# Kernel optimization log

Hardware: AMD Instinct MI355X
Metric: run time of the kernel (lower is better)

Reference implementation:

```python
import jax, jax.numpy as jnp
import numpy as np

N = 100000   # nodes
E = 800000   # edges (avg degree 8)
C = 64       # channels
IN_A = 512
IN_V = 512
EPS = 1e-5
BN_SCALE = float(1.0 / np.sqrt(1.0 + EPS))  # eval-mode BN with rm=0, rv=1


def setup_inputs() -> dict:
    key = jax.random.key(0)
    ks = jax.random.split(key, 24)
    s = 0.05
    rnd = lambda k, shp: jax.random.normal(k, shp, jnp.float32)
    inp = {}
    inp["x"] = rnd(ks[0], (N, 2, IN_A))
    inp["edge_index"] = jax.random.randint(ks[1], (2, E), 0, N, dtype=jnp.int32)
    inp["edge_delta"] = jax.random.randint(ks[2], (E,), 0, 30, dtype=jnp.int32)
    inp["edge_self"] = jax.random.randint(ks[3], (E,), 0, 2, dtype=jnp.int32)
    inp["audio_node_mask"] = (jnp.arange(N) % 2) == 0
    # layer_0 linear projections
    inp["W0a"] = rnd(ks[4], (IN_A, C)) * s
    inp["b0a"] = rnd(ks[5], (C,)) * s
    inp["W0v"] = rnd(ks[6], (IN_V, C)) * s
    inp["b0v"] = rnd(ks[7], (C,)) * s
    # batch_0 affine
    inp["bn0_g"] = 1.0 + rnd(ks[8], (C,)) * s
    inp["bn0_b"] = rnd(ks[9], (C,)) * s
    # 4 EdgeConv LinearPathPreact blocks (stacked along leading axis)
    inp["ec_bn1_g"] = 1.0 + rnd(ks[10], (4, 2 * C)) * s
    inp["ec_bn1_b"] = rnd(ks[11], (4, 2 * C)) * s
    inp["ec_fc1_W"] = rnd(ks[12], (4, 2 * C, C)) * s
    inp["ec_bn2_g"] = 1.0 + rnd(ks[13], (4, C)) * s
    inp["ec_bn2_b"] = rnd(ks[14], (4, C)) * s
    inp["ec_fc2_W"] = rnd(ks[15], (4, C, C)) * s
    # batch_1..batch_3 affines
    inp["bn_g"] = 1.0 + rnd(ks[16], (3, C)) * s
    inp["bn_b"] = rnd(ks[17], (3, C)) * s
    # heads
    inp["fca_W"] = rnd(ks[18], (C, 2)) * s
    inp["fca_b"] = rnd(ks[19], (2,)) * s
    inp["fcv_W"] = rnd(ks[20], (C, 2)) * s
    inp["fcv_b"] = rnd(ks[21], (2,)) * s
    inp["fc_W"] = rnd(ks[22], (C, 2)) * s
    inp["fc_b"] = rnd(ks[23], (2,)) * s
    return inp


def _bn(x, g, b):
    # eval-mode BatchNorm1d with running_mean=0, running_var=1
    return x * (BN_SCALE * g) + b


def _lpp(m, g1, b1, W1, g2, b2, W2):
    # LinearPathPreact: BN -> ReLU -> Linear -> BN -> ReLU -> Linear (no biases)
    h = jnp.maximum(_bn(m, g1, b1), 0.0) @ W1
    return jnp.maximum(_bn(h, g2, b2), 0.0) @ W2


def _edgeconv(xf, src, dst, maskf, g1, b1, W1, g2, b2, W2):
    # PyG EdgeConv: message = nn(cat([x_i, x_j - x_i])), mean-aggregated at dst i.
    # Distance-mask is applied as a 0/1 edge weight with masked mean (no dynamic shapes).
    xi = xf[dst]              # [E, C]
    xj = xf[src]              # [E, C]
    msg = _lpp(jnp.concatenate([xi, xj - xi], axis=-1), g1, b1, W1, g2, b2, W2)
    msg = msg * maskf[:, None]
    cnt = jax.ops.segment_sum(maskf, dst, num_segments=N)
    acc = jax.ops.segment_sum(msg, dst, num_segments=N)
    return acc / jnp.maximum(cnt, 1.0)[:, None]


def reference(x, edge_index, edge_delta, edge_self, audio_node_mask,
              W0a, b0a, W0v, b0v, bn0_g, bn0_b,
              ec_bn1_g, ec_bn1_b, ec_fc1_W, ec_bn2_g, ec_bn2_b, ec_fc2_W,
              bn_g, bn_b, fca_W, fca_b, fcv_W, fcv_b, fc_W, fc_b):
    src, dst = edge_index[0], edge_index[1]
    # only the first two distance masks are used in the original forward
    m1 = (edge_delta < 1).astype(x.dtype)
    m2 = (((edge_delta >= 1) & (edge_delta < 4)) | (edge_self == 1)).astype(x.dtype)

    a_out = x[:, 0, :IN_A] @ W0a + b0a
    v_out = x[:, 1, :IN_V] @ W0v + b0v
    gf = jnp.where(audio_node_mask[:, None], a_out, v_out)
    gf = jnp.maximum(_bn(gf, bn0_g, bn0_b), 0.0)

    def block(xin, k):
        p = (ec_bn1_g[k], ec_bn1_b[k], ec_fc1_W[k], ec_bn2_g[k], ec_bn2_b[k], ec_fc2_W[k])
        h = _edgeconv(xin, src, dst, m1, *p)
        return _edgeconv(h, src, dst, m2, *p)

    g1 = jnp.maximum(_bn(block(gf, 0), bn_g[0], bn_b[0]), 0.0)   # dropout is eval-mode identity
    g2 = jnp.maximum(_bn(block(g1, 1) + g1, bn_g[1], bn_b[1]), 0.0)
    g3 = jnp.maximum(_bn(block(g2, 2) + g2, bn_g[2], bn_b[2]), 0.0)
    g4 = block(g3, 3) + g3

    out = g4 @ fc_W + fc_b
    audio_out = gf[audio_node_mask] @ fca_W + fca_b
    video_out = gf[~audio_node_mask] @ fcv_W + fcv_b
    return (out, audio_out, video_out)
```

## Files before the change

### kernel.cpp

```cpp
#include <hip/hip_runtime.h>


#define NN 100000
#define NE 800000
#define NB 391
#define BNS 0.9999950000374998f

typedef __attribute__((ext_vector_type(8))) short short8;
typedef __attribute__((ext_vector_type(4))) float f32x4;

__device__ __forceinline__ float bf_lo(unsigned u){ union{unsigned i; float f;} v; v.i = u << 16; return v.f; }
__device__ __forceinline__ float bf_hi(unsigned u){ union{unsigned i; float f;} v; v.i = u & 0xffff0000u; return v.f; }
__device__ __forceinline__ float bf2f(unsigned short u){ union{unsigned i; float f;} v; v.i = ((unsigned)u) << 16; return v.f; }
__device__ __forceinline__ unsigned short f2bf(float f){
  union{float f; unsigned i;} v; v.f = f;
  unsigned r = v.i + 0x7fffu + ((v.i >> 16) & 1u);
  return (unsigned short)(r >> 16);
}
__device__ __forceinline__ unsigned packbf(float a, float b){
  return (unsigned)f2bf(a) | ((unsigned)f2bf(b) << 16);
}


__global__ __launch_bounds__(256) void hist_kernel(
    const int* __restrict__ ei, const int* __restrict__ edel,
    const int* __restrict__ esel, int* cnt1, int* cnt2)
{
  int e = blockIdx.x * 256 + threadIdx.x;
  if (e >= NE) return;
  int d = edel[e], s = esel[e], dst = ei[NE + e];
  if (d < 1) atomicAdd(cnt1 + dst, 1);
  if ((d >= 1 && d < 4) || s == 1) atomicAdd(cnt2 + dst, 1);
}

__global__ __launch_bounds__(256) void scan1_kernel(
    const int* __restrict__ cnt1, const int* __restrict__ cnt2,
    int* row1, int* row2, int* bsum)
{
  const int a = blockIdx.y;
  const int* cnt = a ? cnt2 : cnt1;
  int* row = a ? row2 : row1;
  int t = threadIdx.x, b = blockIdx.x, i = b * 256 + t;
  int v = (i < NN) ? cnt[i] : 0;
  __shared__ int sc[256];
  sc[t] = v; __syncthreads();
#pragma unroll
  for (int off = 1; off < 256; off <<= 1){
    int x = (t >= off) ? sc[t - off] : 0;
    __syncthreads();
    sc[t] += x;
    __syncthreads();
  }
  if (i < NN) row[i] = sc[t] - v;
  if (t == 255) bsum[a * 400 + b] = sc[t];
}

__global__ __launch_bounds__(512) void scan2_kernel(int* bsum, int* boff, int* ctr)
{
  int t = threadIdx.x;
  __shared__ int sc[512];
  for (int a = 0; a < 2; a++){
    int v = (t < NB) ? bsum[a * 400 + t] : 0;
    __syncthreads();
    sc[t] = v; __syncthreads();
#pragma unroll
    for (int off = 1; off < 512; off <<= 1){
      int x = (t >= off) ? sc[t - off] : 0;
      __syncthreads();
      sc[t] += x;
      __syncthreads();
    }
    if (t < NB) boff[a * 400 + t] = sc[t] - v;
    if (t == NB - 1) ctr[a] = sc[t];
  }
}

__global__ __launch_bounds__(256) void scan3_kernel(
    int* row1, int* row2, int* cur1, int* cur2, const int* __restrict__ boff)
{
  const int a = blockIdx.y;
  int* row = a ? row2 : row1;
  int* cur = a ? cur2 : cur1;
  int i = blockIdx.x * 256 + threadIdx.x;
  if (i >= NN) return;
  int r = row[i] + boff[a * 400 + blockIdx.x];
  row[i] = r;
  cur[i] = r;
}

__global__ __launch_bounds__(256) void inv_kernel(
    const int* __restrict__ cnt1, const int* __restrict__ cnt2,
    float* inv1, float* inv2)
{
  int i = blockIdx.x * 256 + threadIdx.x;
  if (i >= NN) return;
  inv1[i] = 1.f / fmaxf((float)cnt1[i], 1.f);
  inv2[i] = 1.f / fmaxf((float)cnt2[i], 1.f);
}

__global__ __launch_bounds__(256) void compact_kernel(
    const int* __restrict__ ei, const int* __restrict__ edel,
    const int* __restrict__ esel, int* cur1, int* cur2,
    int* s1s, int* s2s)
{
  int e = blockIdx.x * 256 + threadIdx.x;
  if (e >= NE) return;
  int d = edel[e], s = esel[e], src = ei[e], dst = ei[NE + e];
  int rec = src | ((dst & 15) << 20);
  if (d < 1){ int p = atomicAdd(cur1 + dst, 1); s1s[p] = rec; }
  if ((d >= 1 && d < 4) || s == 1){ int p = atomicAdd(cur2 + dst, 1); s2s[p] = rec; }
}

__global__ __launch_bounds__(256) void prep_w(
    const float* __restrict__ W1, const float* __restrict__ W2,
    const float* __restrict__ g1, const float* __restrict__ g2,
    const float* __restrict__ b1,
    unsigned short* __restrict__ wf1, unsigned short* __restrict__ wf2,
    float* __restrict__ t1p)
{
  int g = blockIdx.x * 256 + threadIdx.x;
  if (g >= 6656) return;
  if (g >= 6144){
    int i = g - 6144;
    int k = i >> 7, c = i & 127;
    t1p[i] = b1[k * 128 + c] / (BNS * g1[k * 128 + c]);
    return;
  }
  int k = g / 1536, r = g % 1536, f = r >> 6, l = r & 63;
  int q = l >> 4, m = l & 15;
  if (f < 16){
    int t = f >> 2, h = f & 3;
    unsigned short* o = wf1 + (((size_t)k * 16 + f) * 64 + l) * 8;
    const float* Wk = W1 + k * 8192;
    int cp = t * 16 + m;
    float cs = BNS * g2[k * 64 + cp];
#pragma unroll
    for (int j = 0; j < 8; j++){
      int kg = h * 32 + q * 8 + j;
      float w, rs;
      if (kg < 64){
        w  = Wk[(64 + kg) * 64 + cp];
        rs = BNS * g1[k * 128 + 64 + kg];
      } else {
        w  = Wk[(kg - 64) * 64 + cp];
        rs = BNS * g1[k * 128 + kg - 64];
      }
      o[j] = f2bf(w * rs * cs);
    }
  } else {
    int f2 = f - 16, t = f2 >> 1, h = f2 & 1;
    unsigned short* o = wf2 + (((size_t)k * 8 + f2) * 64 + l) * 8;
    const float* Wk = W2 + k * 4096;
#pragma unroll
    for (int j = 0; j < 8; j++){
      int kg = h * 32 + q * 8 + j;
      o[j] = f2bf(Wk[kg * 64 + t * 16 + m]);
    }
  }
}

__global__ __launch_bounds__(256) void prep_w0(
    const float* __restrict__ W0a, const float* __restrict__ W0v,
    unsigned short* __restrict__ wf0)
{
  int g = blockIdx.x * 256 + threadIdx.x;
  if (g >= 8192) return;
  int l = g & 63, t = (g >> 6) & 3, ks = (g >> 8) & 15, tt = (g >> 12) & 1;
  const float* W = tt ? W0v : W0a;
  int c = t * 16 + (l & 15);
  int kb = ks * 32 + (l >> 4) * 8;
  unsigned short* o = wf0 + (size_t)g * 8;
#pragma unroll
  for (int j = 0; j < 8; j++) o[j] = f2bf(W[(kb + j) * 64 + c]);
}


__global__ __launch_bounds__(256) void s0_kernel(
    const float* __restrict__ x,
    const float* __restrict__ b0a, const float* __restrict__ b0v,
    const float* __restrict__ bn0g, const float* __restrict__ bn0b,
    const unsigned short* __restrict__ wf0,
    unsigned short* __restrict__ Xb)
{
  const int tt = blockIdx.y;
  const int wv = threadIdx.x >> 6;
  const int l  = threadIdx.x & 63;
  const int q = l >> 4, m16 = l & 15;
  const int wid = blockIdx.x * 4 + wv;
  if (wid >= 3125) return;
  const int node = wid * 16 + m16;
  const float* bias = tt ? b0v : b0a;

  float fs[4][4], ft[4][4];
#pragma unroll
  for (int t = 0; t < 4; t++)
#pragma unroll
    for (int r = 0; r < 4; r++){
      int c = t * 16 + q * 4 + r;
      float s = BNS * bn0g[c];
      fs[t][r] = s;
      ft[t][r] = bias[c] * s + bn0b[c];
    }

  const unsigned short* wbase = wf0 + (size_t)tt * 16 * 4 * 64 * 8;
  const float* xp = x + (size_t)(2 * node + tt) * 1024 + tt * 512 + q * 8;

  f32x4 acc[4];
#pragma unroll
  for (int t = 0; t < 4; t++) acc[t] = (f32x4){0.f, 0.f, 0.f, 0.f};

  for (int ks = 0; ks < 16; ks++){
    float4 xa = *(const float4*)(xp + ks * 32);
    float4 xb = *(const float4*)(xp + ks * 32 + 4);
    union { unsigned u[4]; short8 s; } bb;
    bb.u[0] = packbf(xa.x, xa.y);
    bb.u[1] = packbf(xa.z, xa.w);
    bb.u[2] = packbf(xb.x, xb.y);
    bb.u[3] = packbf(xb.z, xb.w);
    const unsigned short* wk = wbase + (size_t)ks * 4 * 64 * 8 + l * 8;
#pragma unroll
    for (int t = 0; t < 4; t++){
      short8 a = *(const short8*)(wk + t * 64 * 8);
      acc[t] = __builtin_amdgcn_mfma_f32_16x16x32_bf16(a, bb.s, acc[t], 0, 0, 0);
    }
  }

  const int i = 2 * node + tt;
  unsigned short* op = Xb + (size_t)i * 64 + (q << 2);
#pragma unroll
  for (int t = 0; t < 4; t++){
    float v0 = fmaxf(fmaf(acc[t][0], fs[t][0], ft[t][0]), 0.f);
    float v1 = fmaxf(fmaf(acc[t][1], fs[t][1], ft[t][1]), 0.f);
    float v2 = fmaxf(fmaf(acc[t][2], fs[t][2], ft[t][2]), 0.f);
    float v3 = fmaxf(fmaf(acc[t][3], fs[t][3], ft[t][3]), 0.f);
    uint2 w; w.x = packbf(v0, v1); w.y = packbf(v2, v3);
    *(uint2*)(op + t * 16) = w;
  }
}


__global__ __launch_bounds__(256, 3) void edge_pass(
    const unsigned short* __restrict__ fin,
    const int* __restrict__ spk,
    const int* __restrict__ row, const int* __restrict__ cnt,
    const float* __restrict__ inv,
    const unsigned short* __restrict__ wf1,
    const unsigned short* __restrict__ wf2,
    const float* __restrict__ t1p,
    const float* __restrict__ bn2b,
    const unsigned short* resid,
    const float* __restrict__ bng, const float* __restrict__ bnb,
    unsigned short* __restrict__ outb, int hasres, int hasbn)
{
  const int tid = threadIdx.x;
  const int l = tid & 63;
  const int wv = tid >> 6;
  const int q = l >> 4, m16 = l & 15;
  const int ge = l >> 2, gc0 = (l & 3) << 4;

  __shared__ unsigned short wlds[8192];
  __shared__ unsigned short rt_s[4][16 * 136];
  __shared__ unsigned short zt_s[4][16 * 72];
  __shared__ unsigned short xi_s[4][16 * 72];

  {
    const uint4* s4 = (const uint4*)wf1;
    uint4* d4 = (uint4*)wlds;
#pragma unroll
    for (int i = 0; i < 4; i++) d4[tid + 256 * i] = s4[tid + 256 * i];
  }
  __syncthreads();

  int chunk = blockIdx.x * 4 + wv;
  const bool active = chunk < 6250;
  if (chunk > 6249) chunk = 6249;
  const int d0 = chunk << 4;
  const int nd = d0 + ge;

  unsigned short* rt = rt_s[wv];
  unsigned short* zt = zt_s[wv];
  unsigned short* xi = xi_s[wv];

  const int rlo = row[nd], deg = cnt[nd];
  const float ivd = inv[nd];

  float t1a[16], t1b[16];
#pragma unroll
  for (int j0 = 0; j0 < 16; j0 += 4){
    *(float4*)(t1a + j0) = *(const float4*)(t1p + gc0 + j0);
    *(float4*)(t1b + j0) = *(const float4*)(t1p + 64 + gc0 + j0);
  }
  f32x4 t2v[4];
#pragma unroll
  for (int t = 0; t < 4; t++)
    t2v[t] = *(const f32x4*)(bn2b + t * 16 + (q << 2));

  {
    const uint4* px = (const uint4*)(fin + (size_t)nd * 64 + gc0);
    uint4 u0 = px[0], u1 = px[1];
    unsigned short* wr = xi + ge * 72 + gc0;
    *(uint4*)(wr)     = u0;
    *(uint4*)(wr + 8) = u1;
  }

  const int r_begin = __shfl(rlo, 0);
  const int r_end   = __shfl(rlo + deg, 63);

  float s[16];
#pragma unroll
  for (int j = 0; j < 16; j++) s[j] = 0.f;

  __builtin_amdgcn_wave_barrier();

  for (int e0 = r_begin; e0 < r_end; e0 += 16){
    int eg = e0 + ge; if (eg >= r_end) eg = r_end - 1;
    unsigned v = (unsigned)spk[eg];
    int src = v & 0xFFFFF;
    int d15 = (v >> 20) & 15;
    const uint4* ps = (const uint4*)(fin + (size_t)src * 64 + gc0);
    uint4 su0 = ps[0], su1 = ps[1];
    const uint4* pxi = (const uint4*)(xi + d15 * 72 + gc0);
    uint4 xu0 = pxi[0], xu1 = pxi[1];

    unsigned sa[8] = {su0.x,su0.y,su0.z,su0.w,su1.x,su1.y,su1.z,su1.w};
    unsigned xa[8] = {xu0.x,xu0.y,xu0.z,xu0.w,xu1.x,xu1.y,xu1.z,xu1.w};
    unsigned rb[8], rc[8];
#pragma unroll
    for (int p = 0; p < 8; p++){
      float x0 = bf_lo(xa[p]), x1 = bf_hi(xa[p]);
      float e0f = bf_lo(sa[p]) - x0, e1f = bf_hi(sa[p]) - x1;
      rb[p] = packbf(fmaxf(e0f + t1b[2*p], 0.f), fmaxf(e1f + t1b[2*p+1], 0.f));
      rc[p] = packbf(fmaxf(x0 + t1a[2*p], 0.f),  fmaxf(x1 + t1a[2*p+1], 0.f));
    }
    unsigned short* wr = rt + ge * 136 + gc0;
    { uint4 u; u.x=rb[0]; u.y=rb[1]; u.z=rb[2]; u.w=rb[3]; *(uint4*)(wr)      = u; }
    { uint4 u; u.x=rb[4]; u.y=rb[5]; u.z=rb[6]; u.w=rb[7]; *(uint4*)(wr + 8)  = u; }
    { uint4 u; u.x=rc[0]; u.y=rc[1]; u.z=rc[2]; u.w=rc[3]; *(uint4*)(wr + 64) = u; }
    { uint4 u; u.x=rc[4]; u.y=rc[5]; u.z=rc[6]; u.w=rc[7]; *(uint4*)(wr + 72) = u; }

    __builtin_amdgcn_wave_barrier();

    const unsigned short* rrow = rt + m16 * 136 + q * 8;
    short8 b1[4];
#pragma unroll
    for (int h = 0; h < 4; h++) b1[h] = *(const short8*)(rrow + h * 32);

#pragma unroll
    for (int t = 0; t < 4; t++){
      f32x4 c = {0.f, 0.f, 0.f, 0.f};
#pragma unroll
      for (int h = 0; h < 4; h++){
        short8 a = *(const short8*)(wlds + ((t * 4 + h) * 64 + l) * 8);
        c = __builtin_amdgcn_mfma_f32_16x16x32_bf16(a, b1[h], c, 0, 0, 0);
      }
      uint2 w;
      w.x = packbf(fmaxf(c[0] + t2v[t][0], 0.f), fmaxf(c[1] + t2v[t][1], 0.f));
      w.y = packbf(fmaxf(c[2] + t2v[t][2], 0.f), fmaxf(c[3] + t2v[t][3], 0.f));
      *(uint2*)(zt + m16 * 72 + t * 16 + (q << 2)) = w;
    }

    __builtin_amdgcn_wave_barrier();

    int jlo = rlo - e0;       if (jlo < 0)  jlo = 0;
    int jhi = rlo + deg - e0; if (jhi > 16) jhi = 16;
    for (int j = jlo; j < jhi; j++){
      const uint4* pz = (const uint4*)(zt + j * 72 + gc0);
      uint4 z0 = pz[0], z1 = pz[1];
      unsigned za[8] = {z0.x,z0.y,z0.z,z0.w,z1.x,z1.y,z1.z,z1.w};
#pragma unroll
      for (int p = 0; p < 8; p++){
        s[2*p]   += bf_lo(za[p]);
        s[2*p+1] += bf_hi(za[p]);
      }
    }
    __builtin_amdgcn_wave_barrier();
  }

  unsigned pk[8];
#pragma unroll
  for (int p = 0; p < 8; p++) pk[p] = packbf(s[2*p] * ivd, s[2*p+1] * ivd);
  unsigned short* wr = zt + ge * 72 + gc0;
  { uint4 u; u.x=pk[0]; u.y=pk[1]; u.z=pk[2]; u.w=pk[3]; *(uint4*)(wr)     = u; }
  { uint4 u; u.x=pk[4]; u.y=pk[5]; u.z=pk[6]; u.w=pk[7]; *(uint4*)(wr + 8) = u; }

  __builtin_amdgcn_wave_barrier();

  short8 a2[4][2];
#pragma unroll
  for (int t = 0; t < 4; t++)
#pragma unroll
    for (int h = 0; h < 2; h++)
      a2[t][h] = *(const short8*)(wf2 + (((size_t)(t * 2 + h)) * 64 + l) * 8);

  const unsigned short* r2row = zt + m16 * 72 + q * 8;
  short8 b2[2];
  b2[0] = *(const short8*)(r2row);
  b2[1] = *(const short8*)(r2row + 32);

  const int dn = d0 + m16;
  unsigned short* op = outb + (size_t)dn * 64 + (q << 2);
#pragma unroll
  for (int t = 0; t < 4; t++){
    f32x4 c = {0.f, 0.f, 0.f, 0.f};
    c = __builtin_amdgcn_mfma_f32_16x16x32_bf16(a2[t][0], b2[0], c, 0, 0, 0);
    c = __builtin_amdgcn_mfma_f32_16x16x32_bf16(a2[t][1], b2[1], c, 0, 0, 0);
    float v0 = c[0], v1 = c[1], v2 = c[2], v3 = c[3];
    if (hasres){
      uint2 rv = *(const uint2*)(resid + (size_t)dn * 64 + t * 16 + (q << 2));
      v0 += bf_lo(rv.x); v1 += bf_hi(rv.x);
      v2 += bf_lo(rv.y); v3 += bf_hi(rv.y);
    }
    if (hasbn){
      f32x4 g = *(const f32x4*)(bng + t * 16 + (q << 2));
      f32x4 b = *(const f32x4*)(bnb + t * 16 + (q << 2));
      v0 = fmaxf(fmaf(v0, BNS * g[0], b[0]), 0.f);
      v1 = fmaxf(fmaf(v1, BNS * g[1], b[1]), 0.f);
      v2 = fmaxf(fmaf(v2, BNS * g[2], b[2]), 0.f);
      v3 = fmaxf(fmaf(v3, BNS * g[3], b[3]), 0.f);
    }
    if (active){
      uint2 w; w.x = packbf(v0, v1); w.y = packbf(v2, v3);
      *(uint2*)(op + t * 16) = w;
    }
  }
}


__global__ __launch_bounds__(256) void head_final(
    const unsigned short* __restrict__ Xb,
    const float* __restrict__ Wf, const float* __restrict__ bf,
    float* __restrict__ out)
{
  int i = (blockIdx.x << 2) + (threadIdx.x >> 6);
  if (i >= NN) return;
  int l = threadIdx.x & 63;
  float v = bf2f(Xb[i * 64 + l]);
  float2 w = *(const float2*)(Wf + l * 2);
  float p0 = v * w.x, p1 = v * w.y;
#pragma unroll
  for (int off = 32; off; off >>= 1){
    p0 += __shfl_xor(p0, off);
    p1 += __shfl_xor(p1, off);
  }
  if (l == 0){ out[i * 2] = p0 + bf[0]; out[i * 2 + 1] = p1 + bf[1]; }
}

__global__ __launch_bounds__(256) void head_av(
    const unsigned short* __restrict__ Xb,
    const float* __restrict__ Wa, const float* __restrict__ ba,
    const float* __restrict__ Wv, const float* __restrict__ bv,
    float* __restrict__ outA, float* __restrict__ outV)
{
  int i = (blockIdx.x << 2) + (threadIdx.x >> 6);
  if (i >= NN) return;
  int l = threadIdx.x & 63;
  const float* Wf = (i & 1) ? Wv : Wa;
  const float* bb = (i & 1) ? bv : ba;
  float* o = (i & 1) ? (outV + (i >> 1) * 2) : (outA + (i >> 1) * 2);
  float v = bf2f(Xb[i * 64 + l]);
  float2 w = *(const float2*)(Wf + l * 2);
  float p0 = v * w.x, p1 = v * w.y;
#pragma unroll
  for (int off = 32; off; off >>= 1){
    p0 += __shfl_xor(p0, off);
    p1 += __shfl_xor(p1, off);
  }
  if (l == 0){ o[0] = p0 + bb[0]; o[1] = p1 + bb[1]; }
}


extern "C" void kernel_launch(void* const* d_in, const int* in_sizes, int n_in,
                              void* d_out, int out_size, void* d_ws, size_t ws_size,
                              hipStream_t stream)
{
  const float* x    = (const float*)d_in[0];
  const int*   ei   = (const int*)d_in[1];
  const int*   edel = (const int*)d_in[2];
  const int*   esel = (const int*)d_in[3];
  const float* W0a  = (const float*)d_in[5];
  const float* b0a  = (const float*)d_in[6];
  const float* W0v  = (const float*)d_in[7];
  const float* b0v  = (const float*)d_in[8];
  const float* bn0g = (const float*)d_in[9];
  const float* bn0b = (const float*)d_in[10];
  const float* ec1g = (const float*)d_in[11];
  const float* ec1b = (const float*)d_in[12];
  const float* ecW1 = (const float*)d_in[13];
  const float* ec2g = (const float*)d_in[14];
  const float* ec2b = (const float*)d_in[15];
  const float* ecW2 = (const float*)d_in[16];
  const float* bng  = (const float*)d_in[17];
  const float* bnb  = (const float*)d_in[18];
  const float* fcaW = (const float*)d_in[19];
  const float* fcab = (const float*)d_in[20];
  const float* fcvW = (const float*)d_in[21];
  const float* fcvb = (const float*)d_in[22];
  const float* fcW  = (const float*)d_in[23];
  const float* fcb  = (const float*)d_in[24];
  float* out = (float*)d_out;

  char* ws = (char*)d_ws;
  unsigned short* Xb   = (unsigned short*)(ws + 102400000);
  unsigned short* Yb   = (unsigned short*)(ws + 115200000);
  int*            s1s  = (int*)(ws + 128000000);
  int*            s2s  = (int*)(ws + 134400000);
  int*            cnt1 = (int*)(ws + 140800000);
  int*            cnt2 = (int*)(ws + 141200000);
  int*            row1 = (int*)(ws + 141600000);
  int*            row2 = (int*)(ws + 142000000);
  int*            cur1 = (int*)(ws + 142400000);
  int*            cur2 = (int*)(ws + 142800000);
  float*          inv1 = (float*)(ws + 143200000);
  float*          inv2 = (float*)(ws + 143600000);
  int*            bsum = (int*)(ws + 144000000);
  int*            boff = (int*)(ws + 144003200);
  int*            ctr  = (int*)(ws + 144006400);
  unsigned short* wf1  = (unsigned short*)(ws + 144006464);
  unsigned short* wf2  = (unsigned short*)(ws + 144137536);
  float*          t1p  = (float*)(ws + 144203072);
  unsigned short* wf0  = (unsigned short*)(ws + 0);

  hipMemsetAsync(cnt1, 0, 800000, stream);

  hist_kernel<<<(NE + 255) / 256, 256, 0, stream>>>(ei, edel, esel, cnt1, cnt2);
  scan1_kernel<<<dim3(NB, 2), 256, 0, stream>>>(cnt1, cnt2, row1, row2, bsum);
  scan2_kernel<<<1, 512, 0, stream>>>(bsum, boff, ctr);
  scan3_kernel<<<dim3(NB, 2), 256, 0, stream>>>(row1, row2, cur1, cur2, boff);
  inv_kernel<<<NB, 256, 0, stream>>>(cnt1, cnt2, inv1, inv2);
  compact_kernel<<<(NE + 255) / 256, 256, 0, stream>>>(ei, edel, esel, cur1, cur2,
                                                       s1s, s2s);
  prep_w<<<26, 256, 0, stream>>>(ecW1, ecW2, ec1g, ec2g, ec1b, wf1, wf2, t1p);
  prep_w0<<<32, 256, 0, stream>>>(W0a, W0v, wf0);

  s0_kernel<<<dim3(782, 2), 256, 0, stream>>>(x, b0a, b0v, bn0g, bn0b, wf0, Xb);
  head_av<<<25000, 256, 0, stream>>>(Xb, fcaW, fcab, fcvW, fcvb,
                                     out + 2 * NN, out + 2 * NN + 100000);

  const int EGB = 1563;

  for (int k = 0; k < 4; k++){
    const unsigned short* w1k = wf1 + (size_t)k * 16 * 64 * 8;
    const unsigned short* w2k = wf2 + (size_t)k * 8 * 64 * 8;
    const float* t1k = t1p + k * 128;
    const float* b2p = ec2b + k * 64;

    edge_pass<<<EGB, 256, 0, stream>>>(Xb, s1s, row1, cnt1, inv1, w1k, w2k,
                                       t1k, b2p, nullptr, nullptr, nullptr,
                                       Yb, 0, 0);
    const unsigned short* resid = (k == 0) ? nullptr : Xb;
    const float* bg = (k < 3) ? (bng + k * 64) : nullptr;
    const float* bb = (k < 3) ? (bnb + k * 64) : nullptr;
    edge_pass<<<EGB, 256, 0, stream>>>(Yb, s2s, row2, cnt2, inv2, w1k, w2k,
                                       t1k, b2p, resid, bg, bb,
                                       Xb, (k == 0) ? 0 : 1, (k < 3) ? 1 : 0);
  }

  head_final<<<25000, 256, 0, stream>>>(Xb, fcW, fcb, out);
}
```

Baseline: 940.0 us.

## Fuse head projections into producers, merge prep kernels, prefetch edge gathers

The audio/video heads are computed in the s0 epilogue, and the final head is computed in the last edge_pass epilogue, which now skips writing Xb. This removes two 25000-block head kernels and one feature write/read round trip. The inv and prep_w0 kernels are folded into scan3 and prep_all to cut launches. The edge_pass loop also prefetches the next edge index and source row one iteration ahead, which hides gather latency at the cost of extra registers.

```diff
diff --git a/kernel.cpp b/kernel.cpp
--- a/kernel.cpp
+++ b/kernel.cpp
@@ -76,7 +76,9 @@
 }
 
 __global__ __launch_bounds__(256) void scan3_kernel(
-    int* row1, int* row2, int* cur1, int* cur2, const int* __restrict__ boff)
+    int* row1, int* row2, int* cur1, int* cur2, const int* __restrict__ boff,
+    const int* __restrict__ cnt1, const int* __restrict__ cnt2,
+    float* inv1, float* inv2)
 {
   const int a = blockIdx.y;
   int* row = a ? row2 : row1;
@@ -86,16 +88,8 @@
   int r = row[i] + boff[a * 400 + blockIdx.x];
   row[i] = r;
   cur[i] = r;
-}
-
-__global__ __launch_bounds__(256) void inv_kernel(
-    const int* __restrict__ cnt1, const int* __restrict__ cnt2,
-    float* inv1, float* inv2)
-{
-  int i = blockIdx.x * 256 + threadIdx.x;
-  if (i >= NN) return;
-  inv1[i] = 1.f / fmaxf((float)cnt1[i], 1.f);
-  inv2[i] = 1.f / fmaxf((float)cnt2[i], 1.f);
+  if (a == 0) inv1[i] = 1.f / fmaxf((float)cnt1[i], 1.f);
+  else        inv2[i] = 1.f / fmaxf((float)cnt2[i], 1.f);
 }
 
 __global__ __launch_bounds__(256) void compact_kernel(
@@ -111,15 +105,27 @@
   if ((d >= 1 && d < 4) || s == 1){ int p = atomicAdd(cur2 + dst, 1); s2s[p] = rec; }
 }
 
-__global__ __launch_bounds__(256) void prep_w(
+__global__ __launch_bounds__(256) void prep_all(
     const float* __restrict__ W1, const float* __restrict__ W2,
     const float* __restrict__ g1, const float* __restrict__ g2,
     const float* __restrict__ b1,
+    const float* __restrict__ W0a, const float* __restrict__ W0v,
     unsigned short* __restrict__ wf1, unsigned short* __restrict__ wf2,
-    float* __restrict__ t1p)
+    float* __restrict__ t1p, unsigned short* __restrict__ wf0)
 {
   int g = blockIdx.x * 256 + threadIdx.x;
-  if (g >= 6656) return;
+  if (g >= 14848) return;
+  if (g >= 6656){
+    int gg = g - 6656;
+    int l = gg & 63, t = (gg >> 6) & 3, ks = (gg >> 8) & 15, tt = (gg >> 12) & 1;
+    const float* W = tt ? W0v : W0a;
+    int c = t * 16 + (l & 15);
+    int kb = ks * 32 + (l >> 4) * 8;
+    unsigned short* o = wf0 + (size_t)gg * 8;
+#pragma unroll
+    for (int j = 0; j < 8; j++) o[j] = f2bf(W[(kb + j) * 64 + c]);
+    return;
+  }
   if (g >= 6144){
     int i = g - 6144;
     int k = i >> 7, c = i & 127;
@@ -159,28 +165,16 @@
   }
 }
 
-__global__ __launch_bounds__(256) void prep_w0(
-    const float* __restrict__ W0a, const float* __restrict__ W0v,
-    unsigned short* __restrict__ wf0)
-{
-  int g = blockIdx.x * 256 + threadIdx.x;
-  if (g >= 8192) return;
-  int l = g & 63, t = (g >> 6) & 3, ks = (g >> 8) & 15, tt = (g >> 12) & 1;
-  const float* W = tt ? W0v : W0a;
-  int c = t * 16 + (l & 15);
-  int kb = ks * 32 + (l >> 4) * 8;
-  unsigned short* o = wf0 + (size_t)g * 8;
-#pragma unroll
-  for (int j = 0; j < 8; j++) o[j] = f2bf(W[(kb + j) * 64 + c]);
-}
-
 
 __global__ __launch_bounds__(256) void s0_kernel(
     const float* __restrict__ x,
     const float* __restrict__ b0a, const float* __restrict__ b0v,
     const float* __restrict__ bn0g, const float* __restrict__ bn0b,
     const unsigned short* __restrict__ wf0,
-    unsigned short* __restrict__ Xb)
+    const float* __restrict__ fcaW, const float* __restrict__ fcab,
+    const float* __restrict__ fcvW, const float* __restrict__ fcvb,
+    unsigned short* __restrict__ Xb, float* __restrict__ outA,
+    float* __restrict__ outV)
 {
   const int tt = blockIdx.y;
   const int wv = threadIdx.x >> 6;
@@ -190,6 +184,7 @@
   if (wid >= 3125) return;
   const int node = wid * 16 + m16;
   const float* bias = tt ? b0v : b0a;
+  const float* WH = tt ? fcvW : fcaW;
 
   float fs[4][4], ft[4][4];
 #pragma unroll
@@ -202,7 +197,7 @@
       ft[t][r] = bias[c] * s + bn0b[c];
     }
 
-  const unsigned short* wbase = wf0 + (size_t)tt * 16 * 4 * 64 * 8;
+  const unsigned short* wbase = wf0 + (size_t)tt * 32768;
   const float* xp = x + (size_t)(2 * node + tt) * 1024 + tt * 512 + q * 8;
 
   f32x4 acc[4];
@@ -212,29 +207,44 @@
   for (int ks = 0; ks < 16; ks++){
     float4 xa = *(const float4*)(xp + ks * 32);
     float4 xb = *(const float4*)(xp + ks * 32 + 4);
-    union { unsigned u[4]; short8 s; } bb;
-    bb.u[0] = packbf(xa.x, xa.y);
-    bb.u[1] = packbf(xa.z, xa.w);
-    bb.u[2] = packbf(xb.x, xb.y);
-    bb.u[3] = packbf(xb.z, xb.w);
-    const unsigned short* wk = wbase + (size_t)ks * 4 * 64 * 8 + l * 8;
+    union { unsigned u4[4]; short8 s8; } bb;
+    bb.u4[0] = packbf(xa.x, xa.y);
+    bb.u4[1] = packbf(xa.z, xa.w);
+    bb.u4[2] = packbf(xb.x, xb.y);
+    bb.u4[3] = packbf(xb.z, xb.w);
+    const unsigned short* wk = wbase + (size_t)ks * 2048 + l * 8;
 #pragma unroll
     for (int t = 0; t < 4; t++){
-      short8 a = *(const short8*)(wk + t * 64 * 8);
-      acc[t] = __builtin_amdgcn_mfma_f32_16x16x32_bf16(a, bb.s, acc[t], 0, 0, 0);
-    }
-  }
-
-  const int i = 2 * node + tt;
-  unsigned short* op = Xb + (size_t)i * 64 + (q << 2);
+      short8 a = *(const short8*)(wk + t * 512);
+      acc[t] = __builtin_amdgcn_mfma_f32_16x16x32_bf16(a, bb.s8, acc[t], 0, 0, 0);
+    }
+  }
+
+  const int i2 = 2 * node + tt;
+  unsigned short* op = Xb + (size_t)i2 * 64 + (q << 2);
+  float p0 = 0.f, p1 = 0.f;
 #pragma unroll
   for (int t = 0; t < 4; t++){
-    float v0 = fmaxf(fmaf(acc[t][0], fs[t][0], ft[t][0]), 0.f);
-    float v1 = fmaxf(fmaf(acc[t][1], fs[t][1], ft[t][1]), 0.f);
-    float v2 = fmaxf(fmaf(acc[t][2], fs[t][2], ft[t][2]), 0.f);
-    float v3 = fmaxf(fmaf(acc[t][3], fs[t][3], ft[t][3]), 0.f);
-    uint2 w; w.x = packbf(v0, v1); w.y = packbf(v2, v3);
+    float v[4];
+#pragma unroll
+    for (int r = 0; r < 4; r++)
+      v[r] = fmaxf(fmaf(acc[t][r], fs[t][r], ft[t][r]), 0.f);
+    uint2 w; w.x = packbf(v[0], v[1]); w.y = packbf(v[2], v[3]);
     *(uint2*)(op + t * 16) = w;
+#pragma unroll
+    for (int r = 0; r < 4; r++){
+      float2 wh = *(const float2*)(WH + 2 * (t * 16 + q * 4 + r));
+      p0 = fmaf(v[r], wh.x, p0);
+      p1 = fmaf(v[r], wh.y, p1);
+    }
+  }
+  p0 += __shfl_xor(p0, 16); p0 += __shfl_xor(p0, 32);
+  p1 += __shfl_xor(p1, 16); p1 += __shfl_xor(p1, 32);
+  if (q == 0){
+    const float* bh = tt ? fcvb : fcab;
+    float* o = (tt ? outV : outA) + node * 2;
+    o[0] = p0 + bh[0];
+    o[1] = p1 + bh[1];
   }
 }
 
@@ -250,7 +260,9 @@
     const float* __restrict__ bn2b,
     const unsigned short* resid,
     const float* __restrict__ bng, const float* __restrict__ bnb,
-    unsigned short* __restrict__ outb, int hasres, int hasbn)
+    unsigned short* __restrict__ outb, int hasres, int hasbn,
+    const float* __restrict__ fcW, const float* __restrict__ fcb,
+    float* __restrict__ outh, int dohead)
 {
   const int tid = threadIdx.x;
   const int l = tid & 63;
@@ -274,8 +286,8 @@
   int chunk = blockIdx.x * 4 + wv;
   const bool active = chunk < 6250;
   if (chunk > 6249) chunk = 6249;
-  const int d0 = chunk << 4;
-  const int nd = d0 + ge;
+  const int d0c = chunk << 4;
+  const int nd = d0c + ge;
 
   unsigned short* rt = rt_s[wv];
   unsigned short* zt = zt_s[wv];
@@ -312,73 +324,92 @@
 
   __builtin_amdgcn_wave_barrier();
 
-  for (int e0 = r_begin; e0 < r_end; e0 += 16){
-    int eg = e0 + ge; if (eg >= r_end) eg = r_end - 1;
-    unsigned v = (unsigned)spk[eg];
-    int src = v & 0xFFFFF;
-    int d15 = (v >> 20) & 15;
-    const uint4* ps = (const uint4*)(fin + (size_t)src * 64 + gc0);
-    uint4 su0 = ps[0], su1 = ps[1];
-    const uint4* pxi = (const uint4*)(xi + d15 * 72 + gc0);
-    uint4 xu0 = pxi[0], xu1 = pxi[1];
-
-    unsigned sa[8] = {su0.x,su0.y,su0.z,su0.w,su1.x,su1.y,su1.z,su1.w};
-    unsigned xa[8] = {xu0.x,xu0.y,xu0.z,xu0.w,xu1.x,xu1.y,xu1.z,xu1.w};
-    unsigned rb[8], rc[8];
-#pragma unroll
-    for (int p = 0; p < 8; p++){
-      float x0 = bf_lo(xa[p]), x1 = bf_hi(xa[p]);
-      float e0f = bf_lo(sa[p]) - x0, e1f = bf_hi(sa[p]) - x1;
-      rb[p] = packbf(fmaxf(e0f + t1b[2*p], 0.f), fmaxf(e1f + t1b[2*p+1], 0.f));
-      rc[p] = packbf(fmaxf(x0 + t1a[2*p], 0.f),  fmaxf(x1 + t1a[2*p+1], 0.f));
-    }
-    unsigned short* wr = rt + ge * 136 + gc0;
-    { uint4 u; u.x=rb[0]; u.y=rb[1]; u.z=rb[2]; u.w=rb[3]; *(uint4*)(wr)      = u; }
-    { uint4 u; u.x=rb[4]; u.y=rb[5]; u.z=rb[6]; u.w=rb[7]; *(uint4*)(wr + 8)  = u; }
-    { uint4 u; u.x=rc[0]; u.y=rc[1]; u.z=rc[2]; u.w=rc[3]; *(uint4*)(wr + 64) = u; }
-    { uint4 u; u.x=rc[4]; u.y=rc[5]; u.z=rc[6]; u.w=rc[7]; *(uint4*)(wr + 72) = u; }
-
-    __builtin_amdgcn_wave_barrier();
-
-    const unsigned short* rrow = rt + m16 * 136 + q * 8;
-    short8 b1[4];
-#pragma unroll
-    for (int h = 0; h < 4; h++) b1[h] = *(const short8*)(rrow + h * 32);
-
-#pragma unroll
-    for (int t = 0; t < 4; t++){
-      f32x4 c = {0.f, 0.f, 0.f, 0.f};
-#pragma unroll
-      for (int h = 0; h < 4; h++){
-        short8 a = *(const short8*)(wlds + ((t * 4 + h) * 64 + l) * 8);
-        c = __builtin_amdgcn_mfma_f32_16x16x32_bf16(a, b1[h], c, 0, 0, 0);
+  if (r_begin < r_end){
+    int eg0 = r_begin + ge; if (eg0 >= r_end) eg0 = r_end - 1;
+    int vc = spk[eg0];
+    const uint4* pr0 = (const uint4*)(fin + (size_t)(vc & 0xFFFFF) * 64 + gc0);
+    uint4 cA = pr0[0], cB = pr0[1];
+    int vn = vc;
+    if (r_begin + 16 < r_end){
+      int eg1 = r_begin + 16 + ge; if (eg1 >= r_end) eg1 = r_end - 1;
+      vn = spk[eg1];
+    }
+
+    for (int e0 = r_begin; e0 < r_end; e0 += 16){
+      const int d15 = (vc >> 20) & 15;
+      const uint4* pxi = (const uint4*)(xi + d15 * 72 + gc0);
+      uint4 xu0 = pxi[0], xu1 = pxi[1];
+      unsigned sa[8] = {cA.x,cA.y,cA.z,cA.w,cB.x,cB.y,cB.z,cB.w};
+      unsigned xa8[8] = {xu0.x,xu0.y,xu0.z,xu0.w,xu1.x,xu1.y,xu1.z,xu1.w};
+      unsigned rb[8], rc[8];
+#pragma unroll
+      for (int p8 = 0; p8 < 8; p8++){
+        float x0 = bf_lo(xa8[p8]), x1 = bf_hi(xa8[p8]);
+        float e0f = bf_lo(sa[p8]) - x0, e1f = bf_hi(sa[p8]) - x1;
+        rb[p8] = packbf(fmaxf(e0f + t1b[2*p8],   0.f),
+                        fmaxf(e1f + t1b[2*p8+1], 0.f));
+        rc[p8] = packbf(fmaxf(x0 + t1a[2*p8],   0.f),
+                        fmaxf(x1 + t1a[2*p8+1], 0.f));
       }
-      uint2 w;
-      w.x = packbf(fmaxf(c[0] + t2v[t][0], 0.f), fmaxf(c[1] + t2v[t][1], 0.f));
-      w.y = packbf(fmaxf(c[2] + t2v[t][2], 0.f), fmaxf(c[3] + t2v[t][3], 0.f));
-      *(uint2*)(zt + m16 * 72 + t * 16 + (q << 2)) = w;
-    }
-
-    __builtin_amdgcn_wave_barrier();
-
-    int jlo = rlo - e0;       if (jlo < 0)  jlo = 0;
-    int jhi = rlo + deg - e0; if (jhi > 16) jhi = 16;
-    for (int j = jlo; j < jhi; j++){
-      const uint4* pz = (const uint4*)(zt + j * 72 + gc0);
-      uint4 z0 = pz[0], z1 = pz[1];
-      unsigned za[8] = {z0.x,z0.y,z0.z,z0.w,z1.x,z1.y,z1.z,z1.w};
-#pragma unroll
-      for (int p = 0; p < 8; p++){
-        s[2*p]   += bf_lo(za[p]);
-        s[2*p+1] += bf_hi(za[p]);
+      unsigned short* wr = rt + ge * 136 + gc0;
+      { uint4 u; u.x=rb[0]; u.y=rb[1]; u.z=rb[2]; u.w=rb[3]; *(uint4*)(wr)      = u; }
+      { uint4 u; u.x=rb[4]; u.y=rb[5]; u.z=rb[6]; u.w=rb[7]; *(uint4*)(wr + 8)  = u; }
+      { uint4 u; u.x=rc[0]; u.y=rc[1]; u.z=rc[2]; u.w=rc[3]; *(uint4*)(wr + 64) = u; }
+      { uint4 u; u.x=rc[4]; u.y=rc[5]; u.z=rc[6]; u.w=rc[7]; *(uint4*)(wr + 72) = u; }
+
+      uint4 nA = cA, nB = cB; int vn2 = vn;
+      if (e0 + 16 < r_end){
+        const uint4* pn = (const uint4*)(fin + (size_t)(vn & 0xFFFFF) * 64 + gc0);
+        nA = pn[0]; nB = pn[1];
+        if (e0 + 32 < r_end){
+          int eg2 = e0 + 32 + ge; if (eg2 >= r_end) eg2 = r_end - 1;
+          vn2 = spk[eg2];
+        }
       }
-    }
-    __builtin_amdgcn_wave_barrier();
+
+      __builtin_amdgcn_wave_barrier();
+
+      const unsigned short* rrow = rt + m16 * 136 + q * 8;
+      short8 b1[4];
+#pragma unroll
+      for (int h = 0; h < 4; h++) b1[h] = *(const short8*)(rrow + h * 32);
+#pragma unroll
+      for (int t = 0; t < 4; t++){
+        f32x4 c = {0.f, 0.f, 0.f, 0.f};
+#pragma unroll
+        for (int h = 0; h < 4; h++){
+          short8 a = *(const short8*)(wlds + ((t * 4 + h) * 64 + l) * 8);
+          c = __builtin_amdgcn_mfma_f32_16x16x32_bf16(a, b1[h], c, 0, 0, 0);
+        }
+        uint2 w;
+        w.x = packbf(fmaxf(c[0] + t2v[t][0], 0.f), fmaxf(c[1] + t2v[t][1], 0.f));
+        w.y = packbf(fmaxf(c[2] + t2v[t][2], 0.f), fmaxf(c[3] + t2v[t][3], 0.f));
+        *(uint2*)(zt + m16 * 72 + t * 16 + (q << 2)) = w;
+      }
+
+      __builtin_amdgcn_wave_barrier();
+
+      int jlo = rlo - e0;       if (jlo < 0)  jlo = 0;
+      int jhi = rlo + deg - e0; if (jhi > 16) jhi = 16;
+      for (int j = jlo; j < jhi; j++){
+        const uint4* pz = (const uint4*)(zt + j * 72 + gc0);
+        uint4 z0 = pz[0], z1 = pz[1];
+        unsigned za[8] = {z0.x,z0.y,z0.z,z0.w,z1.x,z1.y,z1.z,z1.w};
+#pragma unroll
+        for (int p8 = 0; p8 < 8; p8++){
+          s[2*p8]   += bf_lo(za[p8]);
+          s[2*p8+1] += bf_hi(za[p8]);
+        }
+      }
+      __builtin_amdgcn_wave_barrier();
+
+      cA = nA; cB = nB; vc = vn; vn = vn2;
+    }
   }
 
   unsigned pk[8];
 #pragma unroll
-  for (int p = 0; p < 8; p++) pk[p] = packbf(s[2*p] * ivd, s[2*p+1] * ivd);
+  for (int p8 = 0; p8 < 8; p8++) pk[p8] = packbf(s[2*p8] * ivd, s[2*p8+1] * ivd);
   unsigned short* wr = zt + ge * 72 + gc0;
   { uint4 u; u.x=pk[0]; u.y=pk[1]; u.z=pk[2]; u.w=pk[3]; *(uint4*)(wr)     = u; }
   { uint4 u; u.x=pk[4]; u.y=pk[5]; u.z=pk[6]; u.w=pk[7]; *(uint4*)(wr + 8) = u; }
@@ -397,75 +428,47 @@
   b2[0] = *(const short8*)(r2row);
   b2[1] = *(const short8*)(r2row + 32);
 
-  const int dn = d0 + m16;
+  const int dn = d0c + m16;
   unsigned short* op = outb + (size_t)dn * 64 + (q << 2);
+  float p0 = 0.f, p1 = 0.f;
 #pragma unroll
   for (int t = 0; t < 4; t++){
     f32x4 c = {0.f, 0.f, 0.f, 0.f};
     c = __builtin_amdgcn_mfma_f32_16x16x32_bf16(a2[t][0], b2[0], c, 0, 0, 0);
     c = __builtin_amdgcn_mfma_f32_16x16x32_bf16(a2[t][1], b2[1], c, 0, 0, 0);
-    float v0 = c[0], v1 = c[1], v2 = c[2], v3 = c[3];
+    float v[4] = {c[0], c[1], c[2], c[3]};
     if (hasres){
       uint2 rv = *(const uint2*)(resid + (size_t)dn * 64 + t * 16 + (q << 2));
-      v0 += bf_lo(rv.x); v1 += bf_hi(rv.x);
-      v2 += bf_lo(rv.y); v3 += bf_hi(rv.y);
+      v[0] += bf_lo(rv.x); v[1] += bf_hi(rv.x);
+      v[2] += bf_lo(rv.y); v[3] += bf_hi(rv.y);
     }
     if (hasbn){
       f32x4 g = *(const f32x4*)(bng + t * 16 + (q << 2));
       f32x4 b = *(const f32x4*)(bnb + t * 16 + (q << 2));
-      v0 = fmaxf(fmaf(v0, BNS * g[0], b[0]), 0.f);
-      v1 = fmaxf(fmaf(v1, BNS * g[1], b[1]), 0.f);
-      v2 = fmaxf(fmaf(v2, BNS * g[2], b[2]), 0.f);
-      v3 = fmaxf(fmaf(v3, BNS * g[3], b[3]), 0.f);
-    }
-    if (active){
-      uint2 w; w.x = packbf(v0, v1); w.y = packbf(v2, v3);
+#pragma unroll
+      for (int r = 0; r < 4; r++)
+        v[r] = fmaxf(fmaf(v[r], BNS * g[r], b[r]), 0.f);
+    }
+    if (dohead){
+#pragma unroll
+      for (int r = 0; r < 4; r++){
+        float2 wh = *(const float2*)(fcW + 2 * (t * 16 + q * 4 + r));
+        p0 = fmaf(v[r], wh.x, p0);
+        p1 = fmaf(v[r], wh.y, p1);
+      }
+    } else if (active){
+      uint2 w; w.x = packbf(v[0], v[1]); w.y = packbf(v[2], v[3]);
       *(uint2*)(op + t * 16) = w;
     }
   }
-}
-
-
-__global__ __launch_bounds__(256) void head_final(
-    const unsigned short* __restrict__ Xb,
-    const float* __restrict__ Wf, const float* __restrict__ bf,
-    float* __restrict__ out)
-{
-  int i = (blockIdx.x << 2) + (threadIdx.x >> 6);
-  if (i >= NN) return;
-  int l = threadIdx.x & 63;
-  float v = bf2f(Xb[i * 64 + l]);
-  float2 w = *(const float2*)(Wf + l * 2);
-  float p0 = v * w.x, p1 = v * w.y;
-#pragma unroll
-  for (int off = 32; off; off >>= 1){
-    p0 += __shfl_xor(p0, off);
-    p1 += __shfl_xor(p1, off);
-  }
-  if (l == 0){ out[i * 2] = p0 + bf[0]; out[i * 2 + 1] = p1 + bf[1]; }
-}
-
-__global__ __launch_bounds__(256) void head_av(
-    const unsigned short* __restrict__ Xb,
-    const float* __restrict__ Wa, const float* __restrict__ ba,
-    const float* __restrict__ Wv, const float* __restrict__ bv,
-    float* __restrict__ outA, float* __restrict__ outV)
-{
-  int i = (blockIdx.x << 2) + (threadIdx.x >> 6);
-  if (i >= NN) return;
-  int l = threadIdx.x & 63;
-  const float* Wf = (i & 1) ? Wv : Wa;
-  const float* bb = (i & 1) ? bv : ba;
-  float* o = (i & 1) ? (outV + (i >> 1) * 2) : (outA + (i >> 1) * 2);
-  float v = bf2f(Xb[i * 64 + l]);
-  float2 w = *(const float2*)(Wf + l * 2);
-  float p0 = v * w.x, p1 = v * w.y;
-#pragma unroll
-  for (int off = 32; off; off >>= 1){
-    p0 += __shfl_xor(p0, off);
-    p1 += __shfl_xor(p1, off);
-  }
-  if (l == 0){ o[0] = p0 + bb[0]; o[1] = p1 + bb[1]; }
+  if (dohead){
+    p0 += __shfl_xor(p0, 16); p0 += __shfl_xor(p0, 32);
+    p1 += __shfl_xor(p1, 16); p1 += __shfl_xor(p1, 32);
+    if (q == 0 && active){
+      outh[dn * 2]     = p0 + fcb[0];
+      outh[dn * 2 + 1] = p1 + fcb[1];
+    }
+  }
 }
 
 
@@ -498,6 +501,8 @@
   const float* fcW  = (const float*)d_in[23];
   const float* fcb  = (const float*)d_in[24];
   float* out = (float*)d_out;
+  float* outA = out + 2 * NN;
+  float* outV = out + 2 * NN + 100000;
 
   char* ws = (char*)d_ws;
   unsigned short* Xb   = (unsigned short*)(ws + 102400000);
@@ -525,16 +530,16 @@
   hist_kernel<<<(NE + 255) / 256, 256, 0, stream>>>(ei, edel, esel, cnt1, cnt2);
   scan1_kernel<<<dim3(NB, 2), 256, 0, stream>>>(cnt1, cnt2, row1, row2, bsum);
   scan2_kernel<<<1, 512, 0, stream>>>(bsum, boff, ctr);
-  scan3_kernel<<<dim3(NB, 2), 256, 0, stream>>>(row1, row2, cur1, cur2, boff);
-  inv_kernel<<<NB, 256, 0, stream>>>(cnt1, cnt2, inv1, inv2);
+  scan3_kernel<<<dim3(NB, 2), 256, 0, stream>>>(row1, row2, cur1, cur2, boff,
+                                                cnt1, cnt2, inv1, inv2);
   compact_kernel<<<(NE + 255) / 256, 256, 0, stream>>>(ei, edel, esel, cur1, cur2,
                                                        s1s, s2s);
-  prep_w<<<26, 256, 0, stream>>>(ecW1, ecW2, ec1g, ec2g, ec1b, wf1, wf2, t1p);
-  prep_w0<<<32, 256, 0, stream>>>(W0a, W0v, wf0);
-
-  s0_kernel<<<dim3(782, 2), 256, 0, stream>>>(x, b0a, b0v, bn0g, bn0b, wf0, Xb);
-  head_av<<<25000, 256, 0, stream>>>(Xb, fcaW, fcab, fcvW, fcvb,
-                                     out + 2 * NN, out + 2 * NN + 100000);
+  prep_all<<<58, 256, 0, stream>>>(ecW1, ecW2, ec1g, ec2g, ec1b, W0a, W0v,
+                                   wf1, wf2, t1p, wf0);
+
+  s0_kernel<<<dim3(782, 2), 256, 0, stream>>>(x, b0a, b0v, bn0g, bn0b, wf0,
+                                              fcaW, fcab, fcvW, fcvb,
+                                              Xb, outA, outV);
 
   const int EGB = 1563;
 
@@ -546,14 +551,14 @@
 
     edge_pass<<<EGB, 256, 0, stream>>>(Xb, s1s, row1, cnt1, inv1, w1k, w2k,
                                        t1k, b2p, nullptr, nullptr, nullptr,
-                                       Yb, 0, 0);
+                                       Yb, 0, 0, nullptr, nullptr, nullptr, 0);
     const unsigned short* resid = (k == 0) ? nullptr : Xb;
     const float* bg = (k < 3) ? (bng + k * 64) : nullptr;
     const float* bb = (k < 3) ? (bnb + k * 64) : nullptr;
+    const int dohead = (k == 3);
     edge_pass<<<EGB, 256, 0, stream>>>(Yb, s2s, row2, cnt2, inv2, w1k, w2k,
                                        t1k, b2p, resid, bg, bb,
-                                       Xb, (k == 0) ? 0 : 1, (k < 3) ? 1 : 0);
-  }
-
-  head_final<<<25000, 256, 0, stream>>>(Xb, fcW, fcb, out);
-}
+                                       Xb, (k == 0) ? 0 : 1, (k < 3) ? 1 : 0,
+                                       fcW, fcb, out, dohead);
+  }
+}
```

Result: faster. 879.0 us (-6.5%).
